# Performance work log

Hardware: AMD Instinct MI355X
Metric: run time of the kernel (lower is better)

## Reference

```python
import jax, jax.numpy as jnp
import numpy as np

N, E, DIN, HID, HEADS = 50000, 400000, 256, 64, 4
EPS_BN = 1e-5

def setup_inputs() -> dict:
    key = jax.random.key(0)
    ks = jax.random.split(key, 12)
    inp = {}
    inp['x'] = jax.random.normal(ks[0], (N, DIN), dtype=jnp.float32)
    inp['edge_index'] = jax.random.randint(ks[1], (2, E), 0, N, dtype=jnp.int64)
    s = 1.0 / np.sqrt(DIN)
    inp['W1'] = jax.random.uniform(ks[2], (DIN, HEADS * HID), jnp.float32, -s, s)
    inp['a_src1'] = jax.random.normal(ks[3], (HEADS, HID), dtype=jnp.float32) * 0.1
    inp['a_dst1'] = jax.random.normal(ks[4], (HEADS, HID), dtype=jnp.float32) * 0.1
    inp['b1'] = jnp.zeros((HEADS * HID,), jnp.float32)
    inp['bn1_w'] = jnp.ones((HEADS * HID,), jnp.float32)
    inp['bn1_b'] = jnp.zeros((HEADS * HID,), jnp.float32)
    inp['bn1_m'] = jnp.zeros((HEADS * HID,), jnp.float32)
    inp['bn1_v'] = jnp.ones((HEADS * HID,), jnp.float32)
    s2 = 1.0 / np.sqrt(HEADS * HID)
    inp['W2'] = jax.random.uniform(ks[5], (HEADS * HID, HID), jnp.float32, -s2, s2)
    inp['a_src2'] = jax.random.normal(ks[6], (1, HID), dtype=jnp.float32) * 0.1
    inp['a_dst2'] = jax.random.normal(ks[7], (1, HID), dtype=jnp.float32) * 0.1
    inp['b2'] = jnp.zeros((HID,), jnp.float32)
    inp['bn2_w'] = jnp.ones((HID,), jnp.float32)
    inp['bn2_b'] = jnp.zeros((HID,), jnp.float32)
    inp['bn2_m'] = jnp.zeros((HID,), jnp.float32)
    inp['bn2_v'] = jnp.ones((HID,), jnp.float32)
    sr = 1.0 / np.sqrt(HID)
    inp['Wr'] = jax.random.uniform(ks[8], (HID, 1), jnp.float32, -sr, sr)
    inp['br'] = jnp.zeros((1,), jnp.float32)
    inp['Wc'] = jax.random.uniform(ks[9], (HID, 1), jnp.float32, -sr, sr)
    inp['bc'] = jnp.zeros((1,), jnp.float32)
    return inp

def gat_layer(x, src, dst, W, a_src, a_dst, bias, concat):
    # x: [N, Fin] -> h: [N, H, D]
    H, D = a_src.shape
    h = (x @ W).reshape(-1, H, D)
    alpha_s = jnp.sum(h * a_src[None], axis=-1)  # [N, H]
    alpha_d = jnp.sum(h * a_dst[None], axis=-1)
    e = jax.nn.leaky_relu(alpha_s[src] + alpha_d[dst], 0.2)  # [Et, H]
    m = jax.ops.segment_max(e, dst, num_segments=N)
    m = jnp.where(jnp.isfinite(m), m, 0.0)
    ex = jnp.exp(e - m[dst])
    denom = jax.ops.segment_sum(ex, dst, num_segments=N)
    alpha = ex / (denom[dst] + 1e-16)  # segment softmax over incoming edges
    msg = h[src] * alpha[:, :, None]  # [Et, H, D]
    out = jax.ops.segment_sum(msg, dst, num_segments=N)  # [N, H, D]
    out = out.reshape(N, H * D) if concat else out.mean(axis=1)
    return out + bias

def batchnorm(x, w, b, mean, var):
    return (x - mean) * jax.lax.rsqrt(var + EPS_BN) * w + b

def reference(x, edge_index, W1, a_src1, a_dst1, b1, bn1_w, bn1_b, bn1_m, bn1_v,
              W2, a_src2, a_dst2, b2, bn2_w, bn2_b, bn2_m, bn2_v, Wr, br, Wc, bc):
    # add self loops (PyG GATConv default)
    loops = jnp.arange(N, dtype=edge_index.dtype)
    src = jnp.concatenate([edge_index[0], loops])
    dst = jnp.concatenate([edge_index[1], loops])
    h = gat_layer(x, src, dst, W1, a_src1, a_dst1, b1, concat=True)
    h = jax.nn.elu(batchnorm(h, bn1_w, bn1_b, bn1_m, bn1_v))
    h = gat_layer(h, src, dst, W2, a_src2, a_dst2, b2, concat=False)
    h = jax.nn.elu(batchnorm(h, bn2_w, bn2_b, bn2_m, bn2_v))
    reg = h @ Wr + br
    clf = jax.nn.sigmoid(h @ Wc + bc)
    return reg, clf
```

## Files before the change

### kernel.cpp

```cpp
#include <hip/hip_runtime.h>
#include <math.h>


typedef unsigned short ushort_t;
typedef unsigned char uchar_t;
typedef __attribute__((ext_vector_type(8))) unsigned short ushort8;
typedef __attribute__((ext_vector_type(4))) unsigned short ushort4v;
typedef __attribute__((ext_vector_type(8))) short short8;
typedef __attribute__((ext_vector_type(4))) float f32x4;
typedef __attribute__((ext_vector_type(2))) float f32x2;

#define EPS_BN 1e-5f

__device__ __forceinline__ ushort_t f2bf(float f) {
  unsigned u = __float_as_uint(f);
  unsigned r = u + 0x7fffu + ((u >> 16) & 1u);
  return (ushort_t)(r >> 16);
}
__device__ __forceinline__ float bf2f(ushort_t h) {
  return __uint_as_float((unsigned)h << 16);
}
__device__ __forceinline__ uchar_t f2fp8(float f) {
  return (uchar_t)(__builtin_amdgcn_cvt_pk_fp8_f32(f, f, 0, false) & 0xff);
}
__device__ __forceinline__ float leaky02(float x) { return x >= 0.f ? x : 0.2f * x; }
__device__ __forceinline__ float elu_fast(float x) {
  return x > 0.f ? x : __expf(x) - 1.f;
}
__device__ __forceinline__ float wave_sum(float v) {
#pragma unroll
  for (int o = 1; o < 64; o <<= 1) v += __shfl_xor(v, o, 64);
  return v;
}
__device__ __forceinline__ int wave_incl_scan(int v, int lane) {
#pragma unroll
  for (int off = 1; off < 64; off <<= 1) {
    int t = __shfl_up(v, off, 64);
    if (lane >= off) v += t;
  }
  return v;
}

__device__ __forceinline__ void gld_lds16(const ushort_t* g, ushort_t* l) {
  __builtin_amdgcn_global_load_lds(
      (const __attribute__((address_space(1))) unsigned int*)g,
      (__attribute__((address_space(3))) unsigned int*)l, 16, 0, 0);
}

__global__ __launch_bounds__(256) void hist_kernel(
    const int* __restrict__ dst, int* __restrict__ counts, int E,
    const float* __restrict__ x, ushort_t* __restrict__ xb, int n8) {
  int e = blockIdx.x * blockDim.x + threadIdx.x;
  if (e < E) atomicAdd(&counts[dst[e]], 1);
  const int gsz = gridDim.x * blockDim.x;
  for (int j = e; j < n8; j += gsz) {
    float4 f0 = *(const float4*)(x + (size_t)j * 8);
    float4 f1 = *(const float4*)(x + (size_t)j * 8 + 4);
    ushort8 u;
    u[0] = f2bf(f0.x); u[1] = f2bf(f0.y); u[2] = f2bf(f0.z); u[3] = f2bf(f0.w);
    u[4] = f2bf(f1.x); u[5] = f2bf(f1.y); u[6] = f2bf(f1.z); u[7] = f2bf(f1.w);
    *(ushort8*)(xb + (size_t)j * 8) = u;
  }
}

__global__ __launch_bounds__(256) void scan_chunks_kernel(
    const int* __restrict__ counts, int* __restrict__ offsets, int* __restrict__ partials,
    int N, int E, int* __restrict__ csr_src,
    const float* __restrict__ W1, const float* __restrict__ W2,
    ushort_t* __restrict__ W1t, ushort_t* __restrict__ W2t,
    const float* __restrict__ b1, const float* __restrict__ bn1w,
    const float* __restrict__ bn1b, const float* __restrict__ bn1m,
    const float* __restrict__ bn1v,
    const float* __restrict__ b2, const float* __restrict__ bn2w,
    const float* __restrict__ bn2b, const float* __restrict__ bn2m,
    const float* __restrict__ bn2v,
    float* __restrict__ S1, float* __restrict__ T1,
    float* __restrict__ S2, float* __restrict__ T2) {
  __shared__ int ws[4];
  const int tid = threadIdx.x, lane = tid & 63, wv = tid >> 6;
  const int i = blockIdx.x * 256 + tid;
  const int gsz = gridDim.x * 256;
  int v = (i < N) ? counts[i] : 0;
  int incl = wave_incl_scan(v, lane);
  if (lane == 63) ws[wv] = incl;
  __syncthreads();
  int wbase = 0;
  for (int k = 0; k < wv; ++k) wbase += ws[k];
  if (i < N) offsets[i] = wbase + incl - v;
  if (tid == 255) partials[blockIdx.x] = wbase + incl;

  for (int j = i; j < 256 * 256; j += gsz) {
    int k = j >> 8, n2 = j & 255;
    W1t[n2 * 256 + k] = f2bf(W1[j]);
  }
  for (int j = i; j < 256 * 64; j += gsz) {
    int k = j >> 6, n2 = j & 63;
    W2t[n2 * 256 + k] = f2bf(W2[j]);
  }
  if (i < 256) {
    float s = bn1w[i] * rsqrtf(bn1v[i] + EPS_BN);
    S1[i] = s;
    T1[i] = (b1[i] - bn1m[i]) * s + bn1b[i];
  } else if (i < 320) {
    int j = i - 256;
    float s = bn2w[j] * rsqrtf(bn2v[j] + EPS_BN);
    S2[j] = s;
    T2[j] = (b2[j] - bn2m[j]) * s + bn2b[j];
  } else if (i < 384) {
    csr_src[E + i - 320] = 0;
  }
}

__global__ __launch_bounds__(256) void scatter_kernel(
    const int* __restrict__ src, const int* __restrict__ dst,
    const int* __restrict__ offsets, const int* __restrict__ partials,
    int* __restrict__ cursor, int* __restrict__ csr_src,
    int* __restrict__ offs2, int E, int N, int nb) {
  __shared__ int pp[256];
  __shared__ int ws[4];
  __shared__ int tot;
  const int tid = threadIdx.x, lane = tid & 63, wv = tid >> 6;
  int v = (tid < nb) ? partials[tid] : 0;
  int incl = wave_incl_scan(v, lane);
  if (lane == 63) ws[wv] = incl;
  __syncthreads();
  int wbase = 0;
  for (int k = 0; k < wv; ++k) wbase += ws[k];
  pp[tid] = wbase + incl - v;
  if (tid == 255) tot = wbase + incl;
  __syncthreads();

  int idx = blockIdx.x * 256 + tid;
  if (idx < E) {
    int d = dst[idx];
    int p = atomicAdd(&cursor[d], 1);
    csr_src[offsets[d] + pp[d >> 8] + p] = src[idx];
  }
  if (idx <= N) {
    offs2[idx] = (idx < N) ? offsets[idx] + pp[idx >> 8] : tot;
  }
}

template <int H, int OUT8, int SWZ>
__global__ __launch_bounds__(256) void gemm_fullk(
    const ushort_t* __restrict__ Ain, const ushort_t* __restrict__ Bt,
    void* __restrict__ Cout, const float* __restrict__ avs, const float* __restrict__ avd,
    float* __restrict__ as_out, float* __restrict__ ad_out, int M) {
  constexpr int NT = H * 64;
  __shared__ ushort_t As[64 * 256];
  __shared__ ushort_t Bs[64 * 256];
  const int t = threadIdx.x;
  const int w = t >> 6, l = t & 63;

  int id = blockIdx.x;
  if (SWZ) {
    const int nwg = gridDim.x;
    const int q = nwg >> 3, rm = nwg & 7;
    int xcd = id & 7, idx = id >> 3;
    id = (xcd < rm ? xcd * (q + 1) : rm * (q + 1) + (xcd - rm) * q) + idx;
  }
  const int mt = (H == 1) ? id : (id >> 2);
  const int head = (H == 1) ? 0 : (id & 3);
  const int m0 = mt * 64;

  {
    const int slot = l & 7;
#pragma unroll
    for (int i = 0; i < 8; ++i) {
      const int r = w * 64 + i * 8 + (l >> 3);
      const int ir = r >> 2, kb = r & 3;
      const int kc = (slot ^ (ir & 7)) << 3;
      const int brow = head * 64 + ir;
      gld_lds16(Bt + (size_t)brow * 256 + kb * 64 + kc,
                &Bs[w * 4096 + i * 512]);
    }
#pragma unroll
    for (int i = 0; i < 8; ++i) {
      const int r = w * 64 + i * 8 + (l >> 3);
      const int ir = r >> 2, kb = r & 3;
      const int kc = (slot ^ (ir & 7)) << 3;
      const int arow = min(m0 + ir, M - 1);
      gld_lds16(Ain + (size_t)arow * 256 + kb * 64 + kc,
                &As[w * 4096 + i * 512]);
    }
  }
  asm volatile("s_waitcnt vmcnt(8)" ::: "memory");
  __builtin_amdgcn_s_barrier();
  asm volatile("s_waitcnt vmcnt(0)" ::: "memory");
  __builtin_amdgcn_sched_barrier(0);

  f32x4 acc[4];
#pragma unroll
  for (int j = 0; j < 4; ++j) acc[j] = (f32x4){0.f, 0.f, 0.f, 0.f};

  const int fr = l & 15;
  const int kq = (l >> 4) << 3;
  const int fx = (fr & 7) << 3;
  const ushort_t* Ab = &As[(w * 16 + fr) << 8];
  const ushort_t* Bb = &Bs[fr << 8];
#pragma unroll
  for (int k0 = 0; k0 < 256; k0 += 32) {
    const int kabs = k0 + kq;
    const int base = (kabs & ~63) + ((kabs & 63) ^ fx);
    short8 af = *(const short8*)&Ab[base];
#pragma unroll
    for (int j = 0; j < 4; ++j) {
      short8 bf8 = *(const short8*)&Bb[j * 4096 + base];
      acc[j] = __builtin_amdgcn_mfma_f32_16x16x32_bf16(af, bf8, acc[j], 0, 0, 0);
    }
  }

  const int rbase = m0 + w * 16 + (l >> 4) * 4;
  const int cb = head * 64 + fr;
#pragma unroll
  for (int j = 0; j < 4; ++j)
#pragma unroll
    for (int r4 = 0; r4 < 4; ++r4) {
      int row = rbase + r4;
      if (row < M) {
        if (OUT8)
          ((uchar_t*)Cout)[(size_t)row * NT + cb + j * 16] = f2fp8(acc[j][r4]);
        else
          ((ushort_t*)Cout)[(size_t)row * NT + cb + j * 16] = f2bf(acc[j][r4]);
      }
    }

  float asw[4], adw[4];
#pragma unroll
  for (int j = 0; j < 4; ++j) {
    asw[j] = avs[head * 64 + fr + j * 16];
    adw[j] = avd[head * 64 + fr + j * 16];
  }
#pragma unroll
  for (int r4 = 0; r4 < 4; ++r4) {
    float s_ = acc[0][r4] * asw[0] + acc[1][r4] * asw[1] +
               acc[2][r4] * asw[2] + acc[3][r4] * asw[3];
    float d_ = acc[0][r4] * adw[0] + acc[1][r4] * adw[1] +
               acc[2][r4] * adw[2] + acc[3][r4] * adw[3];
#pragma unroll
    for (int o = 1; o < 16; o <<= 1) {
      s_ += __shfl_xor(s_, o, 64);
      d_ += __shfl_xor(d_, o, 64);
    }
    if ((l & 15) == 0) {
      int row = rbase + r4;
      if (row < M) {
        as_out[(size_t)row * H + head] = s_;
        ad_out[(size_t)row * H + head] = d_;
      }
    }
  }
}

__global__ __launch_bounds__(256) void agg1_kernel(
    const uchar_t* __restrict__ h1, const int* __restrict__ offsets,
    const int* __restrict__ csr, const float* __restrict__ as1,
    const float* __restrict__ ad1,
    const float* __restrict__ S1, const float* __restrict__ T1,
    ushort_t* __restrict__ out, int N) {
  __shared__ float ldsW[4][64][4];
  const int wv = threadIdx.x >> 6;
  int n = blockIdx.x * 4 + wv;
  int l = threadIdx.x & 63;
  if (n >= N) return;
  const int hh = l >> 4;
  int off = offsets[n], deg = offsets[n + 1] - off;
  const int* csrp = csr + off;
  const unsigned fb = (unsigned)l << 2;
  float4 adn = *(const float4*)&ad1[n * 4];
  float ad_h = (hh & 2) ? ((hh & 1) ? adn.w : adn.z) : ((hh & 1) ? adn.y : adn.x);

  f32x2 acc0 = {0.f, 0.f}, acc1 = {0.f, 0.f};
  float den = 0.f;

  for (int base = 0; base < deg; base += 64) {
    int cnt = min(64, deg - base);
    int s = 0;
    float4 w4 = make_float4(0.f, 0.f, 0.f, 0.f);
    if (l < cnt) {
      s = csrp[base + l];
      float4 a4 = *(const float4*)&as1[s * 4];
      w4.x = __expf(leaky02(a4.x + adn.x));
      w4.y = __expf(leaky02(a4.y + adn.y));
      w4.z = __expf(leaky02(a4.z + adn.z));
      w4.w = __expf(leaky02(a4.w + adn.w));
    }
    *(float4*)&ldsW[wv][l][0] = w4;
    for (int j = 0; j < cnt; j += 8) {
#pragma unroll
      for (int i = 0; i < 8; ++i) {
        int e = j + i;
        unsigned se = (unsigned)__builtin_amdgcn_readlane(s, e);
        float we = ldsW[wv][e][hh];
        unsigned q = *(const unsigned*)(h1 + (size_t)((se << 8) + fb));
        f32x2 lo = __builtin_amdgcn_cvt_pk_f32_fp8(q, false);
        f32x2 hi = __builtin_amdgcn_cvt_pk_f32_fp8(q, true);
        f32x2 w2 = {we, we};
        acc0 = lo * w2 + acc0;
        acc1 = hi * w2 + acc1;
        den += we;
      }
    }
  }

  float4 asn = *(const float4*)&as1[n * 4];
  float as_h = (hh & 2) ? ((hh & 1) ? asn.w : asn.z) : ((hh & 1) ? asn.y : asn.x);
  float ws = __expf(leaky02(as_h + ad_h));
  {
    unsigned q = *(const unsigned*)(h1 + (size_t)(((unsigned)n << 8) + fb));
    f32x2 lo = __builtin_amdgcn_cvt_pk_f32_fp8(q, false);
    f32x2 hi = __builtin_amdgcn_cvt_pk_f32_fp8(q, true);
    f32x2 w2 = {ws, ws};
    acc0 = lo * w2 + acc0;
    acc1 = hi * w2 + acc1;
  }
  float inv = 1.f / (den + ws + 1e-16f);

  const int c0 = l * 4;
  float4 Sv = *(const float4*)&S1[c0];
  float4 Tv = *(const float4*)&T1[c0];
  float o0 = fmaf(acc0.x, inv * Sv.x, Tv.x);
  float o1 = fmaf(acc0.y, inv * Sv.y, Tv.y);
  float o2 = fmaf(acc1.x, inv * Sv.z, Tv.z);
  float o3 = fmaf(acc1.y, inv * Sv.w, Tv.w);
  ushort4v o4;
  o4[0] = f2bf(elu_fast(o0));
  o4[1] = f2bf(elu_fast(o1));
  o4[2] = f2bf(elu_fast(o2));
  o4[3] = f2bf(elu_fast(o3));
  *(ushort4v*)&out[(size_t)n * 256 + c0] = o4;
}

__global__ __launch_bounds__(256) void agg2_kernel(
    const ushort_t* __restrict__ h2, const int* __restrict__ offsets,
    const int* __restrict__ csr, const float* __restrict__ as2,
    const float* __restrict__ ad2,
    const float* __restrict__ S2, const float* __restrict__ T2,
    const float* __restrict__ Wr, const float* __restrict__ br,
    const float* __restrict__ Wc, const float* __restrict__ bc,
    float* __restrict__ out_reg, float* __restrict__ out_clf, int N) {
  __shared__ float ldsW[4][64];
  __shared__ int ldsS[4][64];
  const int wv = threadIdx.x >> 6;
  int n = blockIdx.x * 4 + wv;
  int l = threadIdx.x & 63;
  if (n >= N) return;
  const int g = l >> 4, ll = l & 15;
  int off = offsets[n], deg = offsets[n + 1] - off;
  const int* csrp = csr + off;
  const size_t hoff = (size_t)ll * 4;
  float adn = ad2[n];

  float acc[4] = {0, 0, 0, 0};
  float ds = 0.f;

  for (int base = 0; base < deg; base += 64) {
    int cnt = min(64, deg - base);
    int s = 0;
    float wv_ = 0.f;
    if (l < cnt) {
      s = csrp[base + l];
      wv_ = __expf(leaky02(as2[s] + adn));
    }
    ldsS[wv][l] = s;
    ldsW[wv][l] = wv_;
    ds += wv_;
    for (int j = 0; j < cnt; j += 16) {
      int e0 = j + g, e1 = j + 4 + g, e2 = j + 8 + g, e3 = j + 12 + g;
      int s0 = ldsS[wv][e0], s1 = ldsS[wv][e1], s2 = ldsS[wv][e2], s3 = ldsS[wv][e3];
      float w0 = ldsW[wv][e0], w1 = ldsW[wv][e1], w2 = ldsW[wv][e2], w3 = ldsW[wv][e3];
      ushort4v r0 = *(const ushort4v*)&h2[(size_t)s0 * 64 + hoff];
      ushort4v r1 = *(const ushort4v*)&h2[(size_t)s1 * 64 + hoff];
      ushort4v r2 = *(const ushort4v*)&h2[(size_t)s2 * 64 + hoff];
      ushort4v r3 = *(const ushort4v*)&h2[(size_t)s3 * 64 + hoff];
#pragma unroll
      for (int k = 0; k < 4; ++k) acc[k] = fmaf(w0, bf2f(r0[k]), acc[k]);
#pragma unroll
      for (int k = 0; k < 4; ++k) acc[k] = fmaf(w1, bf2f(r1[k]), acc[k]);
#pragma unroll
      for (int k = 0; k < 4; ++k) acc[k] = fmaf(w2, bf2f(r2[k]), acc[k]);
#pragma unroll
      for (int k = 0; k < 4; ++k) acc[k] = fmaf(w3, bf2f(r3[k]), acc[k]);
    }
  }
#pragma unroll
  for (int k = 0; k < 4; ++k) {
    acc[k] += __shfl_xor(acc[k], 16, 64);
    acc[k] += __shfl_xor(acc[k], 32, 64);
  }
  float den = wave_sum(ds);
  float ws = __expf(leaky02(as2[n] + adn));
  ushort4v hn = *(const ushort4v*)&h2[(size_t)n * 64 + hoff];
#pragma unroll
  for (int k = 0; k < 4; ++k) acc[k] = fmaf(ws, bf2f(hn[k]), acc[k]);
  float inv = 1.f / (den + ws + 1e-16f);

  int c0 = ll * 4;
  float4 Sv = *(const float4*)&S2[c0];
  float4 Tv = *(const float4*)&T2[c0];
  float4 wr = *(const float4*)&Wr[c0];
  float4 wc = *(const float4*)&Wc[c0];
  float Sf[4] = {Sv.x, Sv.y, Sv.z, Sv.w};
  float Tf[4] = {Tv.x, Tv.y, Tv.z, Tv.w};
  float wrf[4] = {wr.x, wr.y, wr.z, wr.w};
  float wcf[4] = {wc.x, wc.y, wc.z, wc.w};
  float rs = 0.f, cs = 0.f;
#pragma unroll
  for (int q = 0; q < 4; ++q) {
    float o = fmaf(acc[q], inv * Sf[q], Tf[q]);
    o = elu_fast(o);
    rs = fmaf(o, wrf[q], rs);
    cs = fmaf(o, wcf[q], cs);
  }
#pragma unroll
  for (int o = 1; o < 16; o <<= 1) {
    rs += __shfl_xor(rs, o, 64);
    cs += __shfl_xor(cs, o, 64);
  }
  if (l == 0) {
    out_reg[n] = rs + br[0];
    float z = cs + bc[0];
    out_clf[n] = 1.f / (1.f + __expf(-z));
  }
}

extern "C" void kernel_launch(void* const* d_in, const int* in_sizes, int n_in,
                              void* d_out, int out_size, void* d_ws, size_t ws_size,
                              hipStream_t stream) {
  const float* x      = (const float*)d_in[0];
  const int*   ei     = (const int*)d_in[1];
  const float* W1     = (const float*)d_in[2];
  const float* a_src1 = (const float*)d_in[3];
  const float* a_dst1 = (const float*)d_in[4];
  const float* b1     = (const float*)d_in[5];
  const float* bn1w   = (const float*)d_in[6];
  const float* bn1b   = (const float*)d_in[7];
  const float* bn1m   = (const float*)d_in[8];
  const float* bn1v   = (const float*)d_in[9];
  const float* W2     = (const float*)d_in[10];
  const float* a_src2 = (const float*)d_in[11];
  const float* a_dst2 = (const float*)d_in[12];
  const float* b2     = (const float*)d_in[13];
  const float* bn2w   = (const float*)d_in[14];
  const float* bn2b   = (const float*)d_in[15];
  const float* bn2m   = (const float*)d_in[16];
  const float* bn2v   = (const float*)d_in[17];
  const float* Wr     = (const float*)d_in[18];
  const float* br     = (const float*)d_in[19];
  const float* Wc     = (const float*)d_in[20];
  const float* bc     = (const float*)d_in[21];

  const int N = in_sizes[0] / 256;
  const int E = in_sizes[1] / 2;
  const int* srcv = ei;
  const int* dstv = ei + E;

  char* w = (char*)d_ws;
  auto alloc = [&](size_t bytes) {
    char* p = w;
    w += (bytes + 255) & ~(size_t)255;
    return p;
  };
  const int nb = (N + 255) / 256;
  const size_t nbytes_rounded = ((size_t)N * 4 + 255) & ~(size_t)255;
  int* counts    = (int*)alloc((size_t)N * 4);
  int* cursor    = (int*)alloc((size_t)N * 4);
  int* offsets   = (int*)alloc((size_t)N * 4);
  int* offs2     = (int*)alloc((size_t)(N + 1) * 4);
  int* partials  = (int*)alloc((size_t)nb * 4);
  int* csr_src   = (int*)alloc((size_t)(E + 64) * 4);
  float* as1     = (float*)alloc((size_t)N * 4 * 4);
  float* ad1     = (float*)alloc((size_t)N * 4 * 4);
  float* as2     = (float*)alloc((size_t)N * 4);
  float* ad2     = (float*)alloc((size_t)N * 4);
  float* S1      = (float*)alloc(256 * 4);
  float* T1      = (float*)alloc(256 * 4);
  float* S2      = (float*)alloc(64 * 4);
  float* T2      = (float*)alloc(64 * 4);
  ushort_t* W1t  = (ushort_t*)alloc((size_t)256 * 256 * 2);
  ushort_t* W2t  = (ushort_t*)alloc((size_t)64 * 256 * 2);
  ushort_t* xb   = (ushort_t*)alloc((size_t)N * 256 * 2);
  uchar_t* h1b   = (uchar_t*)alloc((size_t)N * 256);
  ushort_t* h1a  = (ushort_t*)alloc((size_t)N * 256 * 2);
  ushort_t* h2b  = (ushort_t*)alloc((size_t)N * 64 * 2);

  float* out_reg = (float*)d_out;

  hipMemsetAsync(counts, 0, nbytes_rounded * 2, stream);
  hist_kernel<<<(E + 255) / 256, 256, 0, stream>>>(dstv, counts, E, x, xb, N * 256 / 8);
  scan_chunks_kernel<<<nb, 256, 0, stream>>>(counts, offsets, partials, N, E, csr_src,
                                             W1, W2, W1t, W2t,
                                             b1, bn1w, bn1b, bn1m, bn1v,
                                             b2, bn2w, bn2b, bn2m, bn2v,
                                             S1, T1, S2, T2);
  {
    int items = max(E, N + 1);
    scatter_kernel<<<(items + 255) / 256, 256, 0, stream>>>(srcv, dstv, offsets, partials,
                                                            cursor, csr_src, offs2, E, N, nb);
  }

  const int nwb = (N + 3) / 4;
  const int mtiles = (N + 63) / 64;

  gemm_fullk<4, 1, 1><<<mtiles * 4, 256, 0, stream>>>(
      xb, W1t, h1b, a_src1, a_dst1, as1, ad1, N);
  agg1_kernel<<<nwb, 256, 0, stream>>>(h1b, offs2, csr_src, as1, ad1, S1, T1, h1a, N);

  gemm_fullk<1, 0, 0><<<mtiles, 256, 0, stream>>>(
      h1a, W2t, h2b, a_src2, a_dst2, as2, ad2, N);
  agg2_kernel<<<nwb, 256, 0, stream>>>(h2b, offs2, csr_src, as2, ad2, S2, T2,
                                       Wr, br, Wc, bc, out_reg, out_reg + N, N);
}
```

Baseline: 264.6 us.

## Fuse fp32-to-bf16 conversion into a persistent layer-1 GEMM with resident W1

Removes the separate x→bf16 conversion pass and the xb intermediate buffer. Layer-1 GEMM becomes a persistent 256-block, 512-thread kernel that keeps all of W1 in LDS, reads fp32 x directly, converts it in registers and prefetches the next 32-row tile while computing. This avoids writing and re-reading a 25MB bf16 copy of x and reloading W1 per tile. In exchange, LDS use per block is large (144KB), which limits occupancy to one block per CU, and tiles are smaller.

After: 253.6 us. -4.2%, faster.

```diff
diff --git a/kernel.cpp b/kernel.cpp
--- a/kernel.cpp
+++ b/kernel.cpp
@@ -48,19 +48,9 @@
 }
 
 __global__ __launch_bounds__(256) void hist_kernel(
-    const int* __restrict__ dst, int* __restrict__ counts, int E,
-    const float* __restrict__ x, ushort_t* __restrict__ xb, int n8) {
+    const int* __restrict__ dst, int* __restrict__ counts, int E) {
   int e = blockIdx.x * blockDim.x + threadIdx.x;
   if (e < E) atomicAdd(&counts[dst[e]], 1);
-  const int gsz = gridDim.x * blockDim.x;
-  for (int j = e; j < n8; j += gsz) {
-    float4 f0 = *(const float4*)(x + (size_t)j * 8);
-    float4 f1 = *(const float4*)(x + (size_t)j * 8 + 4);
-    ushort8 u;
-    u[0] = f2bf(f0.x); u[1] = f2bf(f0.y); u[2] = f2bf(f0.z); u[3] = f2bf(f0.w);
-    u[4] = f2bf(f1.x); u[5] = f2bf(f1.y); u[6] = f2bf(f1.z); u[7] = f2bf(f1.w);
-    *(ushort8*)(xb + (size_t)j * 8) = u;
-  }
 }
 
 __global__ __launch_bounds__(256) void scan_chunks_kernel(
@@ -141,27 +131,135 @@
   }
 }
 
-template <int H, int OUT8, int SWZ>
-__global__ __launch_bounds__(256) void gemm_fullk(
+__global__ __launch_bounds__(512) void gemm1_persist(
+    const float* __restrict__ X, const ushort_t* __restrict__ Bt,
+    uchar_t* __restrict__ Cout, const float* __restrict__ avs,
+    const float* __restrict__ avd,
+    float* __restrict__ as_out, float* __restrict__ ad_out, int M, int ntiles) {
+  __shared__ ushort_t Bs[256 * 256];
+  __shared__ ushort_t As[32 * 256];
+  const int t = threadIdx.x;
+  const int w = t >> 6, l = t & 63;
+  const int wr = w >> 2, wc = w & 3;
+
+#pragma unroll
+  for (int it = 0; it < 16; ++it) {
+    int s = it * 512 + t;
+    int i = s >> 5, sr = s & 31;
+    int kb = sr >> 3, sl8 = sr & 7;
+    int kc = (sl8 ^ (i & 7)) << 3;
+    gld_lds16(Bt + (size_t)i * 256 + kb * 64 + kc, &Bs[s * 8]);
+  }
+
+  const int ar = t >> 4, k0a = (t & 15) * 16;
+  int wd0, wd1;
+  {
+    int k = k0a;
+    wd0 = ar * 256 + (k & ~63) + ((k & 63) ^ ((ar & 7) << 3));
+    k = k0a + 8;
+    wd1 = ar * 256 + (k & ~63) + ((k & 63) ^ ((ar & 7) << 3));
+  }
+  float4 fa0, fa1, fa2, fa3;
+  {
+    const float* src = X + (size_t)min(blockIdx.x * 32 + ar, M - 1) * 256 + k0a;
+    fa0 = *(const float4*)(src);
+    fa1 = *(const float4*)(src + 4);
+    fa2 = *(const float4*)(src + 8);
+    fa3 = *(const float4*)(src + 12);
+  }
+
+  const int fr = l & 15;
+  const int kq = (l >> 4) << 3;
+  const int fx = (fr & 7) << 3;
+  const ushort_t* Ab = &As[(wr * 16 + fr) << 8];
+  const ushort_t* Bb = &Bs[(wc * 64 + fr) << 8];
+
+  float asw[4], adw[4];
+#pragma unroll
+  for (int j = 0; j < 4; ++j) {
+    asw[j] = avs[wc * 64 + fr + j * 16];
+    adw[j] = avd[wc * 64 + fr + j * 16];
+  }
+
+  for (int tile = blockIdx.x; tile < ntiles; tile += 256) {
+    ushort8 u0, u1;
+    u0[0] = f2bf(fa0.x); u0[1] = f2bf(fa0.y); u0[2] = f2bf(fa0.z); u0[3] = f2bf(fa0.w);
+    u0[4] = f2bf(fa1.x); u0[5] = f2bf(fa1.y); u0[6] = f2bf(fa1.z); u0[7] = f2bf(fa1.w);
+    u1[0] = f2bf(fa2.x); u1[1] = f2bf(fa2.y); u1[2] = f2bf(fa2.z); u1[3] = f2bf(fa2.w);
+    u1[4] = f2bf(fa3.x); u1[5] = f2bf(fa3.y); u1[6] = f2bf(fa3.z); u1[7] = f2bf(fa3.w);
+    __syncthreads();
+    *(ushort8*)&As[wd0] = u0;
+    *(ushort8*)&As[wd1] = u1;
+    __syncthreads();
+
+    {
+      int nt_ = tile + 256;
+      if (nt_ < ntiles) {
+        const float* src = X + (size_t)min(nt_ * 32 + ar, M - 1) * 256 + k0a;
+        fa0 = *(const float4*)(src);
+        fa1 = *(const float4*)(src + 4);
+        fa2 = *(const float4*)(src + 8);
+        fa3 = *(const float4*)(src + 12);
+      }
+    }
+
+    f32x4 acc[4];
+#pragma unroll
+    for (int j = 0; j < 4; ++j) acc[j] = (f32x4){0.f, 0.f, 0.f, 0.f};
+#pragma unroll
+    for (int k0 = 0; k0 < 256; k0 += 32) {
+      const int kabs = k0 + kq;
+      const int base = (kabs & ~63) + ((kabs & 63) ^ fx);
+      short8 af = *(const short8*)&Ab[base];
+#pragma unroll
+      for (int j = 0; j < 4; ++j) {
+        short8 bf8 = *(const short8*)&Bb[j * 4096 + base];
+        acc[j] = __builtin_amdgcn_mfma_f32_16x16x32_bf16(af, bf8, acc[j], 0, 0, 0);
+      }
+    }
+
+    const int rbase = tile * 32 + wr * 16 + (l >> 4) * 4;
+#pragma unroll
+    for (int j = 0; j < 4; ++j)
+#pragma unroll
+      for (int r4 = 0; r4 < 4; ++r4) {
+        int row = rbase + r4;
+        if (row < M)
+          Cout[(size_t)row * 256 + wc * 64 + fr + j * 16] = f2fp8(acc[j][r4]);
+      }
+
+#pragma unroll
+    for (int r4 = 0; r4 < 4; ++r4) {
+      float s_ = acc[0][r4] * asw[0] + acc[1][r4] * asw[1] +
+                 acc[2][r4] * asw[2] + acc[3][r4] * asw[3];
+      float d_ = acc[0][r4] * adw[0] + acc[1][r4] * adw[1] +
+                 acc[2][r4] * adw[2] + acc[3][r4] * adw[3];
+#pragma unroll
+      for (int o = 1; o < 16; o <<= 1) {
+        s_ += __shfl_xor(s_, o, 64);
+        d_ += __shfl_xor(d_, o, 64);
+      }
+      if ((l & 15) == 0) {
+        int row = rbase + r4;
+        if (row < M) {
+          as_out[(size_t)row * 4 + wc] = s_;
+          ad_out[(size_t)row * 4 + wc] = d_;
+        }
+      }
+    }
+  }
+}
+
+__global__ __launch_bounds__(256) void gemm2_fullk(
     const ushort_t* __restrict__ Ain, const ushort_t* __restrict__ Bt,
-    void* __restrict__ Cout, const float* __restrict__ avs, const float* __restrict__ avd,
+    ushort_t* __restrict__ Cout, const float* __restrict__ avs,
+    const float* __restrict__ avd,
     float* __restrict__ as_out, float* __restrict__ ad_out, int M) {
-  constexpr int NT = H * 64;
   __shared__ ushort_t As[64 * 256];
   __shared__ ushort_t Bs[64 * 256];
   const int t = threadIdx.x;
   const int w = t >> 6, l = t & 63;
-
-  int id = blockIdx.x;
-  if (SWZ) {
-    const int nwg = gridDim.x;
-    const int q = nwg >> 3, rm = nwg & 7;
-    int xcd = id & 7, idx = id >> 3;
-    id = (xcd < rm ? xcd * (q + 1) : rm * (q + 1) + (xcd - rm) * q) + idx;
-  }
-  const int mt = (H == 1) ? id : (id >> 2);
-  const int head = (H == 1) ? 0 : (id & 3);
-  const int m0 = mt * 64;
+  const int m0 = blockIdx.x * 64;
 
   {
     const int slot = l & 7;
@@ -170,9 +268,7 @@
       const int r = w * 64 + i * 8 + (l >> 3);
       const int ir = r >> 2, kb = r & 3;
       const int kc = (slot ^ (ir & 7)) << 3;
-      const int brow = head * 64 + ir;
-      gld_lds16(Bt + (size_t)brow * 256 + kb * 64 + kc,
-                &Bs[w * 4096 + i * 512]);
+      gld_lds16(Bt + (size_t)ir * 256 + kb * 64 + kc, &Bs[w * 4096 + i * 512]);
     }
 #pragma unroll
     for (int i = 0; i < 8; ++i) {
@@ -180,8 +276,7 @@
       const int ir = r >> 2, kb = r & 3;
       const int kc = (slot ^ (ir & 7)) << 3;
       const int arow = min(m0 + ir, M - 1);
-      gld_lds16(Ain + (size_t)arow * 256 + kb * 64 + kc,
-                &As[w * 4096 + i * 512]);
+      gld_lds16(Ain + (size_t)arow * 256 + kb * 64 + kc, &As[w * 4096 + i * 512]);
     }
   }
   asm volatile("s_waitcnt vmcnt(8)" ::: "memory");
@@ -211,25 +306,20 @@
   }
 
   const int rbase = m0 + w * 16 + (l >> 4) * 4;
-  const int cb = head * 64 + fr;
 #pragma unroll
   for (int j = 0; j < 4; ++j)
 #pragma unroll
     for (int r4 = 0; r4 < 4; ++r4) {
       int row = rbase + r4;
-      if (row < M) {
-        if (OUT8)
-          ((uchar_t*)Cout)[(size_t)row * NT + cb + j * 16] = f2fp8(acc[j][r4]);
-        else
-          ((ushort_t*)Cout)[(size_t)row * NT + cb + j * 16] = f2bf(acc[j][r4]);
-      }
+      if (row < M)
+        Cout[(size_t)row * 64 + fr + j * 16] = f2bf(acc[j][r4]);
     }
 
   float asw[4], adw[4];
 #pragma unroll
   for (int j = 0; j < 4; ++j) {
-    asw[j] = avs[head * 64 + fr + j * 16];
-    adw[j] = avd[head * 64 + fr + j * 16];
+    asw[j] = avs[fr + j * 16];
+    adw[j] = avd[fr + j * 16];
   }
 #pragma unroll
   for (int r4 = 0; r4 < 4; ++r4) {
@@ -245,8 +335,8 @@
     if ((l & 15) == 0) {
       int row = rbase + r4;
       if (row < M) {
-        as_out[(size_t)row * H + head] = s_;
-        ad_out[(size_t)row * H + head] = d_;
+        as_out[row] = s_;
+        ad_out[row] = d_;
       }
     }
   }
@@ -479,7 +569,6 @@
   float* T2      = (float*)alloc(64 * 4);
   ushort_t* W1t  = (ushort_t*)alloc((size_t)256 * 256 * 2);
   ushort_t* W2t  = (ushort_t*)alloc((size_t)64 * 256 * 2);
-  ushort_t* xb   = (ushort_t*)alloc((size_t)N * 256 * 2);
   uchar_t* h1b   = (uchar_t*)alloc((size_t)N * 256);
   ushort_t* h1a  = (ushort_t*)alloc((size_t)N * 256 * 2);
   ushort_t* h2b  = (ushort_t*)alloc((size_t)N * 64 * 2);
@@ -487,7 +576,7 @@
   float* out_reg = (float*)d_out;
 
   hipMemsetAsync(counts, 0, nbytes_rounded * 2, stream);
-  hist_kernel<<<(E + 255) / 256, 256, 0, stream>>>(dstv, counts, E, x, xb, N * 256 / 8);
+  hist_kernel<<<(E + 255) / 256, 256, 0, stream>>>(dstv, counts, E);
   scan_chunks_kernel<<<nb, 256, 0, stream>>>(counts, offsets, partials, N, E, csr_src,
                                              W1, W2, W1t, W2t,
                                              b1, bn1w, bn1b, bn1m, bn1v,
@@ -500,13 +589,14 @@
   }
 
   const int nwb = (N + 3) / 4;
-  const int mtiles = (N + 63) / 64;
-
-  gemm_fullk<4, 1, 1><<<mtiles * 4, 256, 0, stream>>>(
-      xb, W1t, h1b, a_src1, a_dst1, as1, ad1, N);
+  const int ntiles1 = (N + 31) / 32;
+  const int mtiles2 = (N + 63) / 64;
+
+  gemm1_persist<<<256, 512, 0, stream>>>(
+      x, W1t, h1b, a_src1, a_dst1, as1, ad1, N, ntiles1);
   agg1_kernel<<<nwb, 256, 0, stream>>>(h1b, offs2, csr_src, as1, ad1, S1, T1, h1a, N);
 
-  gemm_fullk<1, 0, 0><<<mtiles, 256, 0, stream>>>(
+  gemm2_fullk<<<mtiles2, 256, 0, stream>>>(
       h1a, W2t, h2b, a_src2, a_dst2, as2, ad2, N);
   agg2_kernel<<<nwb, 256, 0, stream>>>(h2b, offs2, csr_src, as2, ad2, S2, T2,
                                        Wr, br, Wc, bc, out_reg, out_reg + N, N);
```
